# Optimization experiments

Hardware: AMD Instinct MI355X
Metric: run time of the kernel (lower is better)

## Reference

```python
import jax, jax.numpy as jnp
import numpy as np
import math


def _local_band_mask(L):
    # window_size = ceil(1.2 * log2(L) / 2); True where attention is DISALLOWED
    w = math.ceil(1.2 * np.log2(L) / 2)
    i = jnp.arange(L)[:, None]
    j = jnp.arange(L)[None, :]
    return jnp.abs(i - j) > w  # [L, L] bool, True outside the band


def setup_inputs() -> dict:
    key = jax.random.key(0)
    kq, kk, kv = jax.random.split(key, 3)
    B, L, H, E = 2, 2048, 8, 64
    return {
        "queries": jax.random.normal(kq, (B, L, H, E), dtype=jnp.float32),
        "keys": jax.random.normal(kk, (B, L, H, E), dtype=jnp.float32),
        "values": jax.random.normal(kv, (B, L, H, E), dtype=jnp.float32),
    }


def reference(queries, keys, values):
    # queries/keys: [B, L, H, E], values: [B, L, H, D]
    B, L, H, E = queries.shape
    scale = 1.0 / math.sqrt(E)
    # scores: [B, H, L, L]
    scores = jnp.einsum("bqhe,bkhe->bhqk", queries, keys) * scale
    mask = _local_band_mask(L)  # [L, L]
    scores = jnp.where(mask[None, None, :, :], -jnp.inf, scores)
    attn = jax.nn.softmax(scores, axis=-1)  # dropout is identity in eval
    # output: [B, L, H, D]
    out = jnp.einsum("bhqk,bkhd->bqhd", attn, values)
    return out
```

## Files before the change

### kernel.cpp

```cpp
#include <hip/hip_runtime.h>
#include <math.h>


constexpr int L_DIM = 2048;
constexpr int H_DIM = 8;
constexpr int E_DIM = 64;
constexpr int W = 7;
constexpr int NK = 2 * W + 1;
constexpr int TQ = 32;
constexpr int HALO = 8;
constexpr int ROWS = TQ + 2 * HALO;
constexpr int NCH = ROWS / 4;

template <int CTRL>
__device__ __forceinline__ float dpp_add(float s) {
  int t = __builtin_amdgcn_mov_dpp(__builtin_bit_cast(int, s), CTRL, 0xF, 0xF, true);
  return s + __builtin_bit_cast(float, t);
}

__global__ __launch_bounds__(512, 8) void local_attn_kernel(
    const float* __restrict__ q,
    const float* __restrict__ k,
    const float* __restrict__ v,
    float* __restrict__ out) {
  __shared__ float ks[ROWS * E_DIM];
  __shared__ float vs[ROWS * E_DIM];

  const int cpx = gridDim.x >> 3;
  const int bid = (blockIdx.x & 7) * cpx + (blockIdx.x >> 3);

  const int tile = bid & (L_DIM / TQ - 1);
  const int bh = bid >> 6;
  const int h = bh & (H_DIM - 1);
  const int b = bh >> 3;
  const int l0 = tile * TQ;

  const int tid = threadIdx.x;
  const int wv = tid >> 6;
  const int lane = tid & 63;
  const int qsub = lane >> 4;
  const int c4 = lane & 15;

  const size_t bhb = (size_t)b * L_DIM * H_DIM + h;

  const int rsub = lane >> 4;
#pragma unroll
  for (int t = 0; t < 3; ++t) {
    const int ch = wv + t * 8;
    const int m = (ch >= NCH) ? 1 : 0;
    const int cc = ch - m * NCH;
    const int rl = cc * 4 + rsub;
    int rg = l0 - HALO + rl;
    rg = rg < 0 ? 0 : (rg > L_DIM - 1 ? L_DIM - 1 : rg);
    const float4 val =
        *(const float4*)((m ? v : k) + ((bhb + (size_t)rg * H_DIM) << 6) + c4 * 4);
    *(float4*)&((m ? vs : ks)[(rl * 16 + (c4 ^ (rl & 7))) * 4]) = val;
  }

  const int l0w = l0 + wv * 4;
  const int l = l0w + qsub;
  float4 q0 = *(const float4*)(q + ((bhb + (size_t)l * H_DIM) << 6) + c4 * 4);
  const float scale = 0.125f;
  q0.x *= scale; q0.y *= scale; q0.z *= scale; q0.w *= scale;

  __syncthreads();

  const int base_rl = wv * 4 + 1 + qsub;
  float sc[NK];
#pragma unroll
  for (int j = 0; j < NK; ++j) {
    const int rl = base_rl + j;
    const float4 k0 = *(const float4*)&ks[(rl * 16 + (c4 ^ (rl & 7))) * 4];
    float s = q0.x * k0.x + q0.y * k0.y + q0.z * k0.z + q0.w * k0.w;
    s = dpp_add<0xB1>(s);
    s = dpp_add<0x4E>(s);
    s = dpp_add<0x141>(s);
    s = dpp_add<0x140>(s);
    const int kk = l0w + qsub - W + j;
    sc[j] = ((unsigned)kk < (unsigned)L_DIM) ? s : -INFINITY;
  }

  float mx = sc[0];
#pragma unroll
  for (int j = 1; j < NK; ++j) mx = fmaxf(mx, sc[j]);
  float den = 0.0f;
#pragma unroll
  for (int j = 0; j < NK; ++j) {
    sc[j] = __expf(sc[j] - mx);
    den += sc[j];
  }
  const float inv = __builtin_amdgcn_rcpf(den);

  float4 a0 = {0.f, 0.f, 0.f, 0.f};
#pragma unroll
  for (int j = 0; j < NK; ++j) {
    const int rl = base_rl + j;
    const float4 v0 = *(const float4*)&vs[(rl * 16 + (c4 ^ (rl & 7))) * 4];
    const float p = sc[j];
    a0.x += p * v0.x; a0.y += p * v0.y; a0.z += p * v0.z; a0.w += p * v0.w;
  }

  float* op = out + ((bhb + (size_t)l * H_DIM) << 6) + c4 * 4;
  a0.x *= inv; a0.y *= inv; a0.z *= inv; a0.w *= inv;
  *(float4*)op = a0;
}

extern "C" void kernel_launch(void* const* d_in, const int* in_sizes, int n_in,
                              void* d_out, int out_size, void* d_ws, size_t ws_size,
                              hipStream_t stream) {
  const float* q = (const float*)d_in[0];
  const float* k = (const float*)d_in[1];
  const float* v = (const float*)d_in[2];
  float* out = (float*)d_out;

  const int B = in_sizes[0] / (L_DIM * H_DIM * E_DIM);
  const int blocks = B * H_DIM * (L_DIM / TQ);

  local_attn_kernel<<<blocks, 512, 0, stream>>>(q, k, v, out);
}
```

Baseline: 12.20 us.

## Process two adjacent queries per thread group and double query tile size

Each 16-lane group now handles two consecutive query rows that share 16 key/value rows, so every K and V shared-memory read is reused for two queries. The query tile grows from 32 to 64 rows, which shrinks the halo share of each K/V load and halves the block count. The cost is more registers per thread (occupancy hint lowered from 8 to 4 blocks) and fewer blocks to spread across CUs.

```diff
diff --git a/kernel.cpp b/kernel.cpp
--- a/kernel.cpp
+++ b/kernel.cpp
@@ -6,11 +6,10 @@
 constexpr int H_DIM = 8;
 constexpr int E_DIM = 64;
 constexpr int W = 7;
-constexpr int NK = 2 * W + 1;
-constexpr int TQ = 32;
+constexpr int NU = 16;
+constexpr int TQ = 64;
 constexpr int HALO = 8;
 constexpr int ROWS = TQ + 2 * HALO;
-constexpr int NCH = ROWS / 4;
 
 template <int CTRL>
 __device__ __forceinline__ float dpp_add(float s) {
@@ -18,7 +17,7 @@
   return s + __builtin_bit_cast(float, t);
 }
 
-__global__ __launch_bounds__(512, 8) void local_attn_kernel(
+__global__ __launch_bounds__(512, 4) void local_attn_kernel(
     const float* __restrict__ q,
     const float* __restrict__ k,
     const float* __restrict__ v,
@@ -30,7 +29,7 @@
   const int bid = (blockIdx.x & 7) * cpx + (blockIdx.x >> 3);
 
   const int tile = bid & (L_DIM / TQ - 1);
-  const int bh = bid >> 6;
+  const int bh = bid >> 5;
   const int h = bh & (H_DIM - 1);
   const int b = bh >> 3;
   const int l0 = tile * TQ;
@@ -38,17 +37,17 @@
   const int tid = threadIdx.x;
   const int wv = tid >> 6;
   const int lane = tid & 63;
-  const int qsub = lane >> 4;
+  const int g = lane >> 4;
   const int c4 = lane & 15;
 
   const size_t bhb = (size_t)b * L_DIM * H_DIM + h;
 
   const int rsub = lane >> 4;
 #pragma unroll
-  for (int t = 0; t < 3; ++t) {
+  for (int t = 0; t < 5; ++t) {
     const int ch = wv + t * 8;
-    const int m = (ch >= NCH) ? 1 : 0;
-    const int cc = ch - m * NCH;
+    const int m = (ch >= 20) ? 1 : 0;
+    const int cc = ch - m * 20;
     const int rl = cc * 4 + rsub;
     int rg = l0 - HALO + rl;
     rg = rg < 0 ? 0 : (rg > L_DIM - 1 ? L_DIM - 1 : rg);
@@ -57,52 +56,68 @@
     *(float4*)&((m ? vs : ks)[(rl * 16 + (c4 ^ (rl & 7))) * 4]) = val;
   }
 
-  const int l0w = l0 + wv * 4;
-  const int l = l0w + qsub;
-  float4 q0 = *(const float4*)(q + ((bhb + (size_t)l * H_DIM) << 6) + c4 * 4);
+  const int lA_loc = wv * 8 + 2 * g;
+  const int lA = l0 + lA_loc;
+  const float* qpA = q + ((bhb + (size_t)lA * H_DIM) << 6) + c4 * 4;
+  float4 qA = *(const float4*)qpA;
+  float4 qB = *(const float4*)(qpA + (H_DIM << 6));
   const float scale = 0.125f;
-  q0.x *= scale; q0.y *= scale; q0.z *= scale; q0.w *= scale;
+  qA.x *= scale; qA.y *= scale; qA.z *= scale; qA.w *= scale;
+  qB.x *= scale; qB.y *= scale; qB.z *= scale; qB.w *= scale;
 
   __syncthreads();
 
-  const int base_rl = wv * 4 + 1 + qsub;
-  float sc[NK];
+  const int base_rl = lA_loc + 1;
+  float scA[NU], scB[NU];
 #pragma unroll
-  for (int j = 0; j < NK; ++j) {
-    const int rl = base_rl + j;
+  for (int i = 0; i < NU; ++i) {
+    const int rl = base_rl + i;
     const float4 k0 = *(const float4*)&ks[(rl * 16 + (c4 ^ (rl & 7))) * 4];
-    float s = q0.x * k0.x + q0.y * k0.y + q0.z * k0.z + q0.w * k0.w;
-    s = dpp_add<0xB1>(s);
-    s = dpp_add<0x4E>(s);
-    s = dpp_add<0x141>(s);
-    s = dpp_add<0x140>(s);
-    const int kk = l0w + qsub - W + j;
-    sc[j] = ((unsigned)kk < (unsigned)L_DIM) ? s : -INFINITY;
+    float sA = qA.x * k0.x + qA.y * k0.y + qA.z * k0.z + qA.w * k0.w;
+    float sB = qB.x * k0.x + qB.y * k0.y + qB.z * k0.z + qB.w * k0.w;
+    sA = dpp_add<0xB1>(sA);   sB = dpp_add<0xB1>(sB);
+    sA = dpp_add<0x4E>(sA);   sB = dpp_add<0x4E>(sB);
+    sA = dpp_add<0x141>(sA);  sB = dpp_add<0x141>(sB);
+    sA = dpp_add<0x140>(sA);  sB = dpp_add<0x140>(sB);
+    const int kk = lA - W + i;
+    const bool inr = (unsigned)kk < (unsigned)L_DIM;
+    scA[i] = (inr && i < 15) ? sA : -INFINITY;
+    scB[i] = (inr && i >= 1) ? sB : -INFINITY;
   }
 
-  float mx = sc[0];
+  float mA = scA[0], mB = scB[1];
 #pragma unroll
-  for (int j = 1; j < NK; ++j) mx = fmaxf(mx, sc[j]);
-  float den = 0.0f;
+  for (int i = 1; i < NU; ++i) mA = fmaxf(mA, scA[i]);
 #pragma unroll
-  for (int j = 0; j < NK; ++j) {
-    sc[j] = __expf(sc[j] - mx);
-    den += sc[j];
+  for (int i = 2; i < NU; ++i) mB = fmaxf(mB, scB[i]);
+  float dA = 0.0f, dB = 0.0f;
+#pragma unroll
+  for (int i = 0; i < NU; ++i) {
+    scA[i] = __expf(scA[i] - mA);
+    dA += scA[i];
+    scB[i] = __expf(scB[i] - mB);
+    dB += scB[i];
   }
-  const float inv = __builtin_amdgcn_rcpf(den);
+  const float invA = __builtin_amdgcn_rcpf(dA);
+  const float invB = __builtin_amdgcn_rcpf(dB);
 
-  float4 a0 = {0.f, 0.f, 0.f, 0.f};
+  float4 aA = {0.f, 0.f, 0.f, 0.f};
+  float4 aB = {0.f, 0.f, 0.f, 0.f};
 #pragma unroll
-  for (int j = 0; j < NK; ++j) {
-    const int rl = base_rl + j;
+  for (int i = 0; i < NU; ++i) {
+    const int rl = base_rl + i;
     const float4 v0 = *(const float4*)&vs[(rl * 16 + (c4 ^ (rl & 7))) * 4];
-    const float p = sc[j];
-    a0.x += p * v0.x; a0.y += p * v0.y; a0.z += p * v0.z; a0.w += p * v0.w;
+    const float pA = scA[i];
+    const float pB = scB[i];
+    aA.x += pA * v0.x; aA.y += pA * v0.y; aA.z += pA * v0.z; aA.w += pA * v0.w;
+    aB.x += pB * v0.x; aB.y += pB * v0.y; aB.z += pB * v0.z; aB.w += pB * v0.w;
   }
 
-  float* op = out + ((bhb + (size_t)l * H_DIM) << 6) + c4 * 4;
-  a0.x *= inv; a0.y *= inv; a0.z *= inv; a0.w *= inv;
-  *(float4*)op = a0;
+  float* opA = out + ((bhb + (size_t)lA * H_DIM) << 6) + c4 * 4;
+  aA.x *= invA; aA.y *= invA; aA.z *= invA; aA.w *= invA;
+  aB.x *= invB; aB.y *= invB; aB.z *= invB; aB.w *= invB;
+  *(float4*)opA = aA;
+  *(float4*)(opA + (H_DIM << 6)) = aB;
 }
 
 extern "C" void kernel_launch(void* const* d_in, const int* in_sizes, int n_in,
```

Result: no change. 12.31 us (+0.9%).
